# Performance work log

Measured on AMD Instinct MI355X. Metric: run time of the kernel, lower is better.

## Reference

```python
import jax, jax.numpy as jnp
import numpy as np

S, C, HD = 2048, 3072, 128
H = C // HD  # 24 heads
EPS = 1e-6


def setup_inputs() -> dict:
    key = jax.random.key(0)
    ks = jax.random.split(key, 12)
    x = jax.random.normal(ks[0], (S, C), dtype=jnp.float32)
    rope = jax.random.normal(ks[1], (S, 1, HD // 2, 2, 2), dtype=jnp.float32)
    w = 0.02
    return {
        "x": x,
        "rope": rope,
        "wq": jax.random.normal(ks[2], (C, C), dtype=jnp.float32) * w,
        "bq": jnp.zeros((C,), dtype=jnp.float32),
        "wk": jax.random.normal(ks[3], (C, C), dtype=jnp.float32) * w,
        "bk": jnp.zeros((C,), dtype=jnp.float32),
        "wv": jax.random.normal(ks[4], (C, C), dtype=jnp.float32) * w,
        "bv": jnp.zeros((C,), dtype=jnp.float32),
        "wo": jax.random.normal(ks[5], (C, C), dtype=jnp.float32) * w,
        "bo": jnp.zeros((C,), dtype=jnp.float32),
        "qn_w": jnp.ones((HD,), dtype=jnp.float32),
        "kn_w": jnp.ones((HD,), dtype=jnp.float32),
    }


def _rmsnorm(t, w):
    # t: [S, H, HD]; normalize over last dim
    ms = jnp.mean(t * t, axis=-1, keepdims=True)
    return t * jax.lax.rsqrt(ms + EPS) * w


def _apply_rotary(t, rope):
    # t: [S, H, HD] -> [S, H, HD//2, 1, 2]; rope: [S, 1, HD//2, 2, 2]
    t_ = t.reshape(S, H, HD // 2, 1, 2)
    out = jnp.sum(rope * t_, axis=-1)  # [S, H, HD//2, 2]
    return out.reshape(S, H, HD)


def reference(x, rope, wq, bq, wk, bk, wv, bv, wo, bo, qn_w, kn_w):
    q = (x @ wq.T + bq).reshape(S, H, HD)
    k = (x @ wk.T + bk).reshape(S, H, HD)
    v = (x @ wv.T + bv).reshape(S, H, HD)
    q = _rmsnorm(q, qn_w)
    k = _rmsnorm(k, kn_w)
    q = _apply_rotary(q, rope)
    k = _apply_rotary(k, rope)
    # dense SDPA: scores [H, S, S]
    scores = jnp.einsum('shd,thd->hst', q, k) / jnp.sqrt(jnp.float32(HD))
    attn = jax.nn.softmax(scores, axis=-1)
    out = jnp.einsum('hst,thd->shd', attn, v).reshape(S, C)
    return out @ wo.T + bo
```

## Files before the change

### kernel.cpp

```cpp
#include <hip/hip_runtime.h>
#include <cstdint>
#include <cstddef>

#define SS 2048
#define CC 3072
#define HDIM 128
#define NH 24

using bf16 = __bf16;
typedef __bf16 bf16x8 __attribute__((ext_vector_type(8)));
typedef float f32x4 __attribute__((ext_vector_type(4)));

typedef const __attribute__((address_space(1))) void* gas1_cvp;
typedef __attribute__((address_space(3))) void* las3_vp;

__device__ __forceinline__ void gll16(const void* g, void* l) {
  __builtin_amdgcn_global_load_lds((gas1_cvp)g, (las3_vp)l, 16, 0, 0);
}

__device__ __forceinline__ bf16x8 cvt8(f32x4 a, f32x4 b) {
  bf16x8 r;
  r[0] = (bf16)a[0]; r[1] = (bf16)a[1]; r[2] = (bf16)a[2]; r[3] = (bf16)a[3];
  r[4] = (bf16)b[0]; r[5] = (bf16)b[1]; r[6] = (bf16)b[2]; r[7] = (bf16)b[3];
  return r;
}

#define NX ((size_t)SS * CC)
#define NW ((size_t)CC * CC)

__global__ __launch_bounds__(256)
void k_cvt(const float* __restrict__ s0, const float* __restrict__ s1,
           const float* __restrict__ s2, const float* __restrict__ s3,
           const float* __restrict__ s4, bf16* __restrict__ dst) {
  const int z = blockIdx.y;
  const float* src = (z == 0) ? s0 : (z == 1) ? s1 : (z == 2) ? s2 : (z == 3) ? s3 : s4;
  const size_t nz = (z == 0) ? NX : NW;
  const size_t base = (z == 0) ? 0 : NX + (size_t)(z - 1) * NW;
  const size_t i = ((size_t)blockIdx.x * 256 + threadIdx.x) * 8;
  if (i < nz) {
    const f32x4 a = *(const f32x4*)(src + i);
    const f32x4 b = *(const f32x4*)(src + i + 4);
    *(bf16x8*)(dst + base + i) = cvt8(a, b);
  }
}

__device__ __forceinline__ void gemm_bt_bf16(const bf16* __restrict__ A,
                                             const bf16* __restrict__ W,
                                             const float* __restrict__ bias,
                                             void* __restrict__ out,
                                             int M, int N, int K, int mode) {
  __shared__ __align__(16) bf16 As[2][128][32];
  __shared__ __align__(16) bf16 Ws[2][128][32];
  const int t = threadIdx.x, wave = t >> 6, lane = t & 63;
  const int m0 = blockIdx.y * 128, n0 = blockIdx.x * 128;
  const int wm = (wave >> 1) * 64, wn = (wave & 1) * 64;
  const int fr = lane & 15, fq = (lane >> 4) * 8;

  f32x4 acc[4][4] = {};

  for (int k0 = 0; k0 < K; k0 += 64) {
    __syncthreads();
#pragma unroll
    for (int it = 0; it < 4; ++it) {
      const int pc = wave * 4 + it;
      const int pl = pc >> 3, rb = pc & 7;
      const int row = rb * 16 + (lane >> 2);
      const int c8 = (lane & 3) * 8;
      gll16(A + (size_t)(m0 + row) * K + k0 + pl * 32 + c8,
            (char*)&As[0][0][0] + pc * 1024);
      gll16(W + (size_t)(n0 + row) * K + k0 + pl * 32 + c8,
            (char*)&Ws[0][0][0] + pc * 1024);
    }
    __syncthreads();
#pragma unroll
    for (int c = 0; c < 2; ++c) {
      bf16x8 a[4], b[4];
#pragma unroll
      for (int i = 0; i < 4; ++i) a[i] = *(const bf16x8*)&As[c][wm + i * 16 + fr][fq];
#pragma unroll
      for (int j = 0; j < 4; ++j) b[j] = *(const bf16x8*)&Ws[c][wn + j * 16 + fr][fq];
#pragma unroll
      for (int i = 0; i < 4; ++i)
#pragma unroll
        for (int j = 0; j < 4; ++j)
          acc[i][j] = __builtin_amdgcn_mfma_f32_16x16x32_bf16(a[i], b[j], acc[i][j], 0, 0, 0);
    }
  }

  const int lr4 = (lane >> 4) * 4;
#pragma unroll
  for (int i = 0; i < 4; ++i) {
#pragma unroll
    for (int j = 0; j < 4; ++j) {
      const int col = n0 + wn + j * 16 + fr;
      const float bb = bias[col];
#pragma unroll
      for (int r = 0; r < 4; ++r) {
        const int row = m0 + wm + i * 16 + lr4 + r;
        const float v = acc[i][j][r] + bb;
        if (mode == 0)
          ((bf16*)out)[((size_t)(col >> 7) * M + row) * 128 + (col & 127)] = (bf16)v;
        else if (mode == 1)
          ((bf16*)out)[(size_t)col * M + row] = (bf16)v;
        else
          ((float*)out)[(size_t)row * N + col] = v;
      }
    }
  }
}

__global__ __launch_bounds__(256, 4)
void k_gemm_qkv_b(const bf16* __restrict__ xb,
                  const bf16* __restrict__ wqb, const bf16* __restrict__ wkb,
                  const bf16* __restrict__ wvb,
                  const float* __restrict__ bq, const float* __restrict__ bk,
                  const float* __restrict__ bv,
                  bf16* __restrict__ Qo, bf16* __restrict__ Ko, bf16* __restrict__ Vo) {
  const int z = blockIdx.z;
  const bf16* W  = (z == 0) ? wqb : (z == 1) ? wkb : wvb;
  const float* B = (z == 0) ? bq : (z == 1) ? bk : bv;
  void* O        = (z == 0) ? (void*)Qo : (z == 1) ? (void*)Ko : (void*)Vo;
  gemm_bt_bf16(xb, W, B, O, SS, CC, CC, (z == 2) ? 1 : 0);
}

__global__ __launch_bounds__(256, 4)
void k_gemm_out_b(const bf16* __restrict__ A, const bf16* __restrict__ wob,
                  const float* __restrict__ bo, float* __restrict__ out) {
  gemm_bt_bf16(A, wob, bo, out, SS, CC, CC, 2);
}

template<int AF32>
__device__ __forceinline__ void gemm_core(const void* __restrict__ Ap,
                                          const float* __restrict__ W,
                                          const float* __restrict__ bias,
                                          void* __restrict__ out,
                                          int M, int N, int K, int mode) {
  __shared__ __align__(16) bf16 As[128][32];
  __shared__ __align__(16) bf16 Ws[128][32];
  const int t = threadIdx.x, wave = t >> 6, lane = t & 63;
  const int m0 = blockIdx.y * 128, n0 = blockIdx.x * 128;
  const int wm = (wave >> 1) * 64, wn = (wave & 1) * 64;
  const int fr = lane & 15, fq = (lane >> 4) * 8;
  const int pi0 = wave * 128 + lane;
  const int pi1 = pi0 + 64;
  const int row0 = pi0 >> 2, c0 = (pi0 & 3) * 8;
  const int row1 = pi1 >> 2, c1 = (pi1 & 3) * 8;

  f32x4 raf0[2], raf1[2], rw0[2], rw1[2];
  bf16x8 rab0, rab1;

  auto issue = [&](int k0) {
    if (AF32) {
      const float* A = (const float*)Ap;
      const float* p0 = A + (size_t)(m0 + row0) * K + k0 + c0;
      raf0[0] = *(const f32x4*)p0; raf0[1] = *(const f32x4*)(p0 + 4);
      const float* p1 = A + (size_t)(m0 + row1) * K + k0 + c1;
      raf1[0] = *(const f32x4*)p1; raf1[1] = *(const f32x4*)(p1 + 4);
    } else {
      const bf16* A = (const bf16*)Ap;
      rab0 = *(const bf16x8*)(A + (size_t)(m0 + row0) * K + k0 + c0);
      rab1 = *(const bf16x8*)(A + (size_t)(m0 + row1) * K + k0 + c1);
    }
    const float* q0 = W + (size_t)(n0 + row0) * K + k0 + c0;
    rw0[0] = *(const f32x4*)q0; rw0[1] = *(const f32x4*)(q0 + 4);
    const float* q1 = W + (size_t)(n0 + row1) * K + k0 + c1;
    rw1[0] = *(const f32x4*)q1; rw1[1] = *(const f32x4*)(q1 + 4);
  };

  f32x4 acc[4][4] = {};
  issue(0);
  for (int k0 = 0; k0 < K; k0 += 32) {
    __syncthreads();
    if (AF32) {
      *(bf16x8*)&As[row0][c0] = cvt8(raf0[0], raf0[1]);
      *(bf16x8*)&As[row1][c1] = cvt8(raf1[0], raf1[1]);
    } else {
      *(bf16x8*)&As[row0][c0] = rab0;
      *(bf16x8*)&As[row1][c1] = rab1;
    }
    *(bf16x8*)&Ws[row0][c0] = cvt8(rw0[0], rw0[1]);
    *(bf16x8*)&Ws[row1][c1] = cvt8(rw1[0], rw1[1]);
    __syncthreads();
    if (k0 + 32 < K) issue(k0 + 32);
    bf16x8 a[4], b[4];
#pragma unroll
    for (int i = 0; i < 4; ++i) a[i] = *(const bf16x8*)&As[wm + i * 16 + fr][fq];
#pragma unroll
    for (int j = 0; j < 4; ++j) b[j] = *(const bf16x8*)&Ws[wn + j * 16 + fr][fq];
#pragma unroll
    for (int i = 0; i < 4; ++i)
#pragma unroll
      for (int j = 0; j < 4; ++j)
        acc[i][j] = __builtin_amdgcn_mfma_f32_16x16x32_bf16(a[i], b[j], acc[i][j], 0, 0, 0);
  }

  const int lr4 = (lane >> 4) * 4;
#pragma unroll
  for (int i = 0; i < 4; ++i) {
#pragma unroll
    for (int j = 0; j < 4; ++j) {
      const int col = n0 + wn + j * 16 + fr;
      const float bb = bias[col];
#pragma unroll
      for (int r = 0; r < 4; ++r) {
        const int row = m0 + wm + i * 16 + lr4 + r;
        const float v = acc[i][j][r] + bb;
        if (mode == 0)
          ((bf16*)out)[((size_t)(col >> 7) * M + row) * 128 + (col & 127)] = (bf16)v;
        else if (mode == 1)
          ((bf16*)out)[(size_t)col * M + row] = (bf16)v;
        else
          ((float*)out)[(size_t)row * N + col] = v;
      }
    }
  }
}

__global__ __launch_bounds__(256, 2)
void k_gemm_qkv_f(const float* __restrict__ x,
                  const float* __restrict__ wq, const float* __restrict__ wk,
                  const float* __restrict__ wv,
                  const float* __restrict__ bq, const float* __restrict__ bk,
                  const float* __restrict__ bv,
                  bf16* __restrict__ Qo, bf16* __restrict__ Ko, bf16* __restrict__ Vo) {
  const int z = blockIdx.z;
  const float* W = (z == 0) ? wq : (z == 1) ? wk : wv;
  const float* B = (z == 0) ? bq : (z == 1) ? bk : bv;
  void* O        = (z == 0) ? (void*)Qo : (z == 1) ? (void*)Ko : (void*)Vo;
  gemm_core<1>(x, W, B, O, SS, CC, CC, (z == 2) ? 1 : 0);
}

__global__ __launch_bounds__(256, 2)
void k_gemm_out_f(const bf16* __restrict__ A, const float* __restrict__ wo,
                  const float* __restrict__ bo, float* __restrict__ out) {
  gemm_core<0>(A, wo, bo, out, SS, CC, CC, 2);
}

__global__ __launch_bounds__(256)
void k_norm_rope(bf16* __restrict__ Q, bf16* __restrict__ K,
                 const float* __restrict__ rope,
                 const float* __restrict__ qw, const float* __restrict__ kw) {
  const int t = threadIdx.x, wave = t >> 6, lane = t & 63;
  const int idx = blockIdx.x * 4 + wave;
  const int s = idx / NH, h = idx % NH;
  const size_t base = ((size_t)h * SS + s) * HDIM + 2 * lane;

  bf16 q2[2], k2[2];
  *(uint32_t*)q2 = *(const uint32_t*)(Q + base);
  *(uint32_t*)k2 = *(const uint32_t*)(K + base);
  const float q0 = (float)q2[0], q1 = (float)q2[1];
  const float k0 = (float)k2[0], k1 = (float)k2[1];
  float sq = q0 * q0 + q1 * q1;
  float sk = k0 * k0 + k1 * k1;
#pragma unroll
  for (int m = 1; m < 64; m <<= 1) {
    sq += __shfl_xor(sq, m);
    sk += __shfl_xor(sk, m);
  }
  const float rq = rsqrtf(sq * (1.0f / 128.0f) + 1e-6f);
  const float rk = rsqrtf(sk * (1.0f / 128.0f) + 1e-6f);

  const float qn0 = q0 * rq * qw[2 * lane], qn1 = q1 * rq * qw[2 * lane + 1];
  const float kn0 = k0 * rk * kw[2 * lane], kn1 = k1 * rk * kw[2 * lane + 1];

  const f32x4 rp = *(const f32x4*)(rope + (size_t)s * 256 + 4 * lane);
  const float r00 = rp[0], r01 = rp[1], r10 = rp[2], r11 = rp[3];

  const float SC = 0.08838834764831845f * 1.44269504088896340f;
  const float oq0 = (r00 * qn0 + r01 * qn1) * SC;
  const float oq1 = (r10 * qn0 + r11 * qn1) * SC;
  const float ok0 = r00 * kn0 + r01 * kn1;
  const float ok1 = r10 * kn0 + r11 * kn1;

  bf16 wq2[2] = {(bf16)oq0, (bf16)oq1};
  bf16 wk2[2] = {(bf16)ok0, (bf16)ok1};
  *(uint32_t*)(Q + base) = *(uint32_t*)wq2;
  *(uint32_t*)(K + base) = *(uint32_t*)wk2;
}

__global__ __launch_bounds__(128, 2)
void k_attn(const bf16* __restrict__ Q, const bf16* __restrict__ Kt,
            const bf16* __restrict__ Vt, bf16* __restrict__ Out) {
  __shared__ __align__(16) bf16 Ks[2][64][128];
  __shared__ __align__(16) bf16 Vs[128][64];
  const int t = threadIdx.x, wave = t >> 6, lane = t & 63;
  const int bx = blockIdx.x;
  const int xg = bx & 7, slot = bx >> 3;
  const int h = xg * 3 + (slot >> 5);
  const int q0 = (slot & 31) * 64;
  const int fr = lane & 15, fq = (lane >> 4) * 8;
  const int g4 = lane >> 4;
  const int wq0 = wave * 32;
  const float FM = 32.0f;

  bf16x8 aq[2][4];
#pragma unroll
  for (int qt = 0; qt < 2; ++qt)
#pragma unroll
    for (int kc = 0; kc < 4; ++kc)
      aq[qt][kc] = *(const bf16x8*)(
          Q + ((size_t)h * SS + q0 + wq0 + qt * 16 + fr) * HDIM + kc * 32 + fq);

  auto stageK = [&](int buf, int k0) {
#pragma unroll
    for (int it = 0; it < 8; ++it) {
      const int pc = wave * 8 + it;
      const int s  = pc * 4 + (lane >> 4);
      const int kp = 32 * ((s >> 4) & 1) + 8 * ((s >> 2) & 3)
                   + 4 * (s >> 5) + (s & 3);
      const int sl = (lane & 15) ^ (s & 7);
      gll16(Kt + ((size_t)h * SS + k0 + kp) * HDIM + sl * 8,
            (char*)&Ks[buf][0][0] + pc * 1024);
    }
  };
  auto stageV = [&](int k0) {
#pragma unroll
    for (int it = 0; it < 8; ++it) {
      const int pc = wave * 8 + it;
      const int d  = pc * 8 + (lane >> 3);
      const int sl = (lane & 7) ^ (d & 7);
      gll16(Vt + ((size_t)h * HDIM + d) * SS + k0 + sl * 8,
            (char*)&Vs[0][0] + pc * 1024);
    }
  };

  f32x4 oacc[2][8] = {};
  float lacc[2] = {0.f, 0.f};

  stageK(0, 0);
  int cur = 0;

  for (int k0 = 0; k0 < SS; k0 += 64) {
    const bool notlast = (k0 + 64 < SS);
    stageV(k0);
    if (notlast) {
      stageK(cur ^ 1, k0 + 64);
      asm volatile("s_waitcnt vmcnt(16)" ::: "memory");
    } else {
      asm volatile("s_waitcnt vmcnt(8)" ::: "memory");
    }
    __builtin_amdgcn_s_barrier();
    __builtin_amdgcn_sched_barrier(0);

    f32x4 sacc[2][4] = {};
#pragma unroll
    for (int kc = 0; kc < 4; ++kc) {
#pragma unroll
      for (int jt = 0; jt < 4; ++jt) {
        const bf16x8 b =
            *(const bf16x8*)&Ks[cur][jt * 16 + fr][((((kc << 2) + g4) ^ (fr & 7)) << 3)];
        sacc[0][jt] = __builtin_amdgcn_mfma_f32_16x16x32_bf16(b, aq[0][kc], sacc[0][jt], 0, 0, 0);
        sacc[1][jt] = __builtin_amdgcn_mfma_f32_16x16x32_bf16(b, aq[1][kc], sacc[1][jt], 0, 0, 0);
      }
    }

    bf16x8 ap[2][2];
#pragma unroll
    for (int qt = 0; qt < 2; ++qt) {
      float pv[4][4];
      float ps = 0.f;
#pragma unroll
      for (int jt = 0; jt < 4; ++jt)
#pragma unroll
        for (int r = 0; r < 4; ++r) {
          pv[jt][r] = exp2f(sacc[qt][jt][r] - FM);
          ps += pv[jt][r];
        }
      lacc[qt] += ps;
#pragma unroll
      for (int kc = 0; kc < 2; ++kc) {
        bf16x8 a;
        a[0] = (bf16)pv[kc][0];     a[1] = (bf16)pv[kc][1];
        a[2] = (bf16)pv[kc][2];     a[3] = (bf16)pv[kc][3];
        a[4] = (bf16)pv[2 + kc][0]; a[5] = (bf16)pv[2 + kc][1];
        a[6] = (bf16)pv[2 + kc][2]; a[7] = (bf16)pv[2 + kc][3];
        ap[qt][kc] = a;
      }
    }

    if (notlast) {
      asm volatile("s_waitcnt vmcnt(8)" ::: "memory");
    } else {
      asm volatile("s_waitcnt vmcnt(0)" ::: "memory");
    }
    __builtin_amdgcn_s_barrier();
    __builtin_amdgcn_sched_barrier(0);

#pragma unroll
    for (int kc = 0; kc < 2; ++kc) {
#pragma unroll
      for (int jd = 0; jd < 8; ++jd) {
        const int d = jd * 16 + fr;
        const bf16x8 b =
            *(const bf16x8*)&Vs[d][((((kc << 2) + g4) ^ (fr & 7)) << 3)];
        oacc[0][jd] = __builtin_amdgcn_mfma_f32_16x16x32_bf16(ap[0][kc], b, oacc[0][jd], 0, 0, 0);
        oacc[1][jd] = __builtin_amdgcn_mfma_f32_16x16x32_bf16(ap[1][kc], b, oacc[1][jd], 0, 0, 0);
      }
    }

    __builtin_amdgcn_s_barrier();
    __builtin_amdgcn_sched_barrier(0);
    cur ^= 1;
  }

#pragma unroll
  for (int qt = 0; qt < 2; ++qt) {
    float l = lacc[qt];
    l += __shfl_xor(l, 16);
    l += __shfl_xor(l, 32);
    const float linv = 1.0f / l;
#pragma unroll
    for (int r = 0; r < 4; ++r) {
      const float inv = __shfl(linv, g4 * 4 + r, 16);
      const int row = q0 + wq0 + qt * 16 + g4 * 4 + r;
#pragma unroll
      for (int jd = 0; jd < 8; ++jd) {
        const int col = h * HDIM + jd * 16 + fr;
        Out[(size_t)row * CC + col] = (bf16)(oacc[qt][jd][r] * inv);
      }
    }
  }
}

extern "C" void kernel_launch(void* const* d_in, const int* in_sizes, int n_in,
                              void* d_out, int out_size, void* d_ws, size_t ws_size,
                              hipStream_t stream) {
  const float* x    = (const float*)d_in[0];
  const float* rope = (const float*)d_in[1];
  const float* wq   = (const float*)d_in[2];
  const float* bq   = (const float*)d_in[3];
  const float* wk   = (const float*)d_in[4];
  const float* bk   = (const float*)d_in[5];
  const float* wv   = (const float*)d_in[6];
  const float* bv   = (const float*)d_in[7];
  const float* wo   = (const float*)d_in[8];
  const float* bo   = (const float*)d_in[9];
  const float* qw   = (const float*)d_in[10];
  const float* kw   = (const float*)d_in[11];

  const size_t need = (4 * NX + 4 * NW) * sizeof(bf16);
  bf16* Vt = (bf16*)d_out;

  if (ws_size >= need) {
    bf16* xb  = (bf16*)d_ws;
    bf16* wqb = xb + NX;
    bf16* wkb = wqb + NW;
    bf16* wvb = wkb + NW;
    bf16* wob = wvb + NW;
    bf16* Qn  = wob + NW;
    bf16* Kn  = Qn + NX;
    bf16* Ao  = Kn + NX;

    k_cvt<<<dim3((unsigned)(NW / 2048), 5), 256, 0, stream>>>(x, wq, wk, wv, wo, xb);
    k_gemm_qkv_b<<<dim3(CC / 128, SS / 128, 3), 256, 0, stream>>>(
        xb, wqb, wkb, wvb, bq, bk, bv, Qn, Kn, Vt);
    k_norm_rope<<<dim3(SS * NH / 4), 256, 0, stream>>>(Qn, Kn, rope, qw, kw);
    k_attn<<<dim3((SS / 64) * NH), 128, 0, stream>>>(Qn, Kn, Vt, Ao);
    k_gemm_out_b<<<dim3(CC / 128, SS / 128), 256, 0, stream>>>(Ao, wob, bo, (float*)d_out);
  } else {
    bf16* Qn = (bf16*)d_ws;
    bf16* Kn = Qn + NX;
    bf16* Ao = Kn + NX;

    k_gemm_qkv_f<<<dim3(CC / 128, SS / 128, 3), 256, 0, stream>>>(
        x, wq, wk, wv, bq, bk, bv, Qn, Kn, Vt);
    k_norm_rope<<<dim3(SS * NH / 4), 256, 0, stream>>>(Qn, Kn, rope, qw, kw);
    k_attn<<<dim3((SS / 64) * NH), 128, 0, stream>>>(Qn, Kn, Vt, Ao);
    k_gemm_out_f<<<dim3(CC / 128, SS / 128), 256, 0, stream>>>(Ao, wo, bo, (float*)d_out);
  }
}
```

Measured before the change: 508.9 us.

## Replace QKV GEMM with 256x256-tile, 8-wave, XOR-swizzled, double-buffered kernel

Adds a new QKV projection kernel that uses 256x256 output tiles with 512 threads (8 waves), 64-wide K steps, XOR-swizzled LDS layout, and interleaves next-tile global-to-LDS loads with MFMA phases under raised wave priority. Larger tiles raise arithmetic intensity and cut redundant global reads. The swizzle avoids LDS bank conflicts. The cost is a big LDS footprint (128KB), high register use for the 8x4 accumulators, and only 288 blocks, which may leave compute units unevenly loaded.

```diff
diff --git a/kernel.cpp b/kernel.cpp
--- a/kernel.cpp
+++ b/kernel.cpp
@@ -44,6 +44,105 @@
   }
 }
 
+__global__ __launch_bounds__(512, 2)
+void k_gemm_qkv_8p(const bf16* __restrict__ xb,
+                   const bf16* __restrict__ wqb, const bf16* __restrict__ wkb,
+                   const bf16* __restrict__ wvb,
+                   const float* __restrict__ bq, const float* __restrict__ bk,
+                   const float* __restrict__ bv,
+                   bf16* __restrict__ Qo, bf16* __restrict__ Ko, bf16* __restrict__ Vo) {
+  const int z = blockIdx.z;
+  const bf16* W   = (z == 0) ? wqb : (z == 1) ? wkb : wvb;
+  const float* Bi = (z == 0) ? bq : (z == 1) ? bk : bv;
+  const int mode  = (z == 2) ? 1 : 0;
+  void* out       = (z == 0) ? (void*)Qo : (z == 1) ? (void*)Ko : (void*)Vo;
+
+  __shared__ __align__(16) bf16 As[2][256][64];
+  __shared__ __align__(16) bf16 Ws[2][256][64];
+  const int t = threadIdx.x, wave = t >> 6, lane = t & 63;
+  const int m0 = blockIdx.y * 256, n0 = blockIdx.x * 256;
+  const int wm = (wave >> 2) * 128, wn = (wave & 3) * 64;
+  const int fr = lane & 15, g4 = lane >> 4;
+  const int K = CC, M = SS;
+
+  auto stage = [&](int buf, int k0, int i) {
+    const int c = wave * 4 + i;
+    const int row = c * 8 + (lane >> 3);
+    const int sl = (lane & 7) ^ (row & 7);
+    gll16(xb + (size_t)(m0 + row) * K + k0 + sl * 8,
+          (char*)&As[buf][0][0] + c * 1024);
+    gll16(W + (size_t)(n0 + row) * K + k0 + sl * 8,
+          (char*)&Ws[buf][0][0] + c * 1024);
+  };
+
+  f32x4 acc[8][4] = {};
+
+  stage(0, 0, 0); stage(0, 0, 1); stage(0, 0, 2); stage(0, 0, 3);
+
+  const int NT = K / 64;
+  for (int tt = 0; tt < NT; ++tt) {
+    const int buf = tt & 1;
+    asm volatile("s_waitcnt vmcnt(0)" ::: "memory");
+    __builtin_amdgcn_s_barrier();
+    __builtin_amdgcn_sched_barrier(0);
+
+    bf16x8 bfr[4][2];
+#pragma unroll
+    for (int ni = 0; ni < 4; ++ni)
+#pragma unroll
+      for (int kk = 0; kk < 2; ++kk) {
+        const int row = wn + ni * 16 + fr;
+        const int sl = (kk * 4 + g4) ^ (row & 7);
+        bfr[ni][kk] = *(const bf16x8*)((const char*)&Ws[buf][0][0] + row * 128 + sl * 16);
+      }
+
+#pragma unroll
+    for (int ph = 0; ph < 4; ++ph) {
+      bf16x8 am[2][2];
+#pragma unroll
+      for (int mi2 = 0; mi2 < 2; ++mi2)
+#pragma unroll
+        for (int kk = 0; kk < 2; ++kk) {
+          const int row = wm + (ph * 2 + mi2) * 16 + fr;
+          const int sl = (kk * 4 + g4) ^ (row & 7);
+          am[mi2][kk] = *(const bf16x8*)((const char*)&As[buf][0][0] + row * 128 + sl * 16);
+        }
+      if (ph < 2 && tt + 1 < NT) {
+        stage(buf ^ 1, (tt + 1) * 64, ph * 2);
+        stage(buf ^ 1, (tt + 1) * 64, ph * 2 + 1);
+      }
+      __builtin_amdgcn_s_setprio(1);
+#pragma unroll
+      for (int kk = 0; kk < 2; ++kk)
+#pragma unroll
+        for (int mi2 = 0; mi2 < 2; ++mi2)
+#pragma unroll
+          for (int ni = 0; ni < 4; ++ni)
+            acc[ph * 2 + mi2][ni] = __builtin_amdgcn_mfma_f32_16x16x32_bf16(
+                am[mi2][kk], bfr[ni][kk], acc[ph * 2 + mi2][ni], 0, 0, 0);
+      __builtin_amdgcn_s_setprio(0);
+    }
+  }
+
+  const int lr4 = g4 * 4;
+#pragma unroll
+  for (int mi = 0; mi < 8; ++mi)
+#pragma unroll
+    for (int ni = 0; ni < 4; ++ni) {
+      const int col = n0 + wn + ni * 16 + fr;
+      const float bb = Bi[col];
+#pragma unroll
+      for (int r = 0; r < 4; ++r) {
+        const int row = m0 + wm + mi * 16 + lr4 + r;
+        const float v = acc[mi][ni][r] + bb;
+        if (mode == 0)
+          ((bf16*)out)[((size_t)(col >> 7) * M + row) * 128 + (col & 127)] = (bf16)v;
+        else
+          ((bf16*)out)[(size_t)col * M + row] = (bf16)v;
+      }
+    }
+}
+
 __device__ __forceinline__ void gemm_bt_bf16(const bf16* __restrict__ A,
                                              const bf16* __restrict__ W,
                                              const float* __restrict__ bias,
@@ -107,20 +206,6 @@
       }
     }
   }
-}
-
-__global__ __launch_bounds__(256, 4)
-void k_gemm_qkv_b(const bf16* __restrict__ xb,
-                  const bf16* __restrict__ wqb, const bf16* __restrict__ wkb,
-                  const bf16* __restrict__ wvb,
-                  const float* __restrict__ bq, const float* __restrict__ bk,
-                  const float* __restrict__ bv,
-                  bf16* __restrict__ Qo, bf16* __restrict__ Ko, bf16* __restrict__ Vo) {
-  const int z = blockIdx.z;
-  const bf16* W  = (z == 0) ? wqb : (z == 1) ? wkb : wvb;
-  const float* B = (z == 0) ? bq : (z == 1) ? bk : bv;
-  void* O        = (z == 0) ? (void*)Qo : (z == 1) ? (void*)Ko : (void*)Vo;
-  gemm_bt_bf16(xb, W, B, O, SS, CC, CC, (z == 2) ? 1 : 0);
 }
 
 __global__ __launch_bounds__(256, 4)
@@ -452,7 +537,7 @@
     bf16* Ao  = Kn + NX;
 
     k_cvt<<<dim3((unsigned)(NW / 2048), 5), 256, 0, stream>>>(x, wq, wk, wv, wo, xb);
-    k_gemm_qkv_b<<<dim3(CC / 128, SS / 128, 3), 256, 0, stream>>>(
+    k_gemm_qkv_8p<<<dim3(CC / 256, SS / 256, 3), 512, 0, stream>>>(
         xb, wqb, wkb, wvb, bq, bk, bv, Qn, Kn, Vt);
     k_norm_rope<<<dim3(SS * NH / 4), 256, 0, stream>>>(Qn, Kn, rope, qw, kw);
     k_attn<<<dim3((SS / 64) * NH), 128, 0, stream>>>(Qn, Kn, Vt, Ao);
```

Measured after the change: 545.3 us. 7.1% more time.

## Fuse RMSNorm and rotary embedding into QKV GEMM epilogue

Applied to the files above, without the earlier changes.

Moves the per-head RMSNorm, rotary application and Q scaling into the epilogue of the bf16 QKV GEMM, so the separate norm/rope kernel launch is dropped on the workspace path. Row sums of squares are reduced across lanes with shuffles, and partial sums from the two N-waves are combined through a small shared array, since each 128-column tile is exactly one head. This removes a full read-modify-write pass over Q and K. In exchange it adds epilogue work, extra rope loads per element and a block barrier inside the GEMM.

```diff
diff --git a/kernel.cpp b/kernel.cpp
--- a/kernel.cpp
+++ b/kernel.cpp
@@ -27,6 +27,7 @@
 
 #define NX ((size_t)SS * CC)
 #define NW ((size_t)CC * CC)
+#define QSCALE (0.08838834764831845f * 1.44269504088896340f)
 
 __global__ __launch_bounds__(256)
 void k_cvt(const float* __restrict__ s0, const float* __restrict__ s1,
@@ -48,9 +49,13 @@
                                              const bf16* __restrict__ W,
                                              const float* __restrict__ bias,
                                              void* __restrict__ out,
-                                             int M, int N, int K, int mode) {
+                                             int M, int N, int K, int mode,
+                                             const float* __restrict__ nw,
+                                             const float* __restrict__ rope_t,
+                                             float scale) {
   __shared__ __align__(16) bf16 As[2][128][32];
   __shared__ __align__(16) bf16 Ws[2][128][32];
+  __shared__ float rs_[4][64];
   const int t = threadIdx.x, wave = t >> 6, lane = t & 63;
   const int m0 = blockIdx.y * 128, n0 = blockIdx.x * 128;
   const int wm = (wave >> 1) * 64, wn = (wave & 1) * 64;
@@ -88,6 +93,60 @@
   }
 
   const int lr4 = (lane >> 4) * 4;
+
+  if (mode == 0) {
+    float bcol[4], nwv[4];
+#pragma unroll
+    for (int j = 0; j < 4; ++j) {
+      bcol[j] = bias[n0 + wn + j * 16 + fr];
+      nwv[j]  = nw[wn + j * 16 + fr];
+    }
+    float ss[4][4];
+#pragma unroll
+    for (int i = 0; i < 4; ++i)
+#pragma unroll
+      for (int r = 0; r < 4; ++r) {
+        float s = 0.f;
+#pragma unroll
+        for (int j = 0; j < 4; ++j) {
+          const float v = acc[i][j][r] + bcol[j];
+          s += v * v;
+        }
+#pragma unroll
+        for (int m = 1; m < 16; m <<= 1) s += __shfl_xor(s, m);
+        ss[i][r] = s;
+      }
+    if (fr == 0) {
+#pragma unroll
+      for (int i = 0; i < 4; ++i)
+#pragma unroll
+        for (int r = 0; r < 4; ++r)
+          rs_[wave][i * 16 + lr4 + r] = ss[i][r];
+    }
+    __syncthreads();
+
+    const int hh = n0 >> 7;
+#pragma unroll
+    for (int i = 0; i < 4; ++i)
+#pragma unroll
+      for (int r = 0; r < 4; ++r) {
+        const float tot = ss[i][r] + rs_[wave ^ 1][i * 16 + lr4 + r];
+        const float rq = rsqrtf(tot * (1.0f / 128.0f) + 1e-6f);
+        const int srow = m0 + wm + i * 16 + lr4 + r;
+#pragma unroll
+        for (int j = 0; j < 4; ++j) {
+          const int d = wn + j * 16 + fr;
+          const float vn = (acc[i][j][r] + bcol[j]) * rq * nwv[j];
+          const float vp = __shfl_xor(vn, 1);
+          const f32x4 rp = *(const f32x4*)(rope_t + (size_t)srow * 256 + (d >> 1) * 4);
+          const float o = ((d & 1) ? (rp[2] * vp + rp[3] * vn)
+                                   : (rp[0] * vn + rp[1] * vp)) * scale;
+          ((bf16*)out)[((size_t)hh * M + srow) * 128 + d] = (bf16)o;
+        }
+      }
+    return;
+  }
+
 #pragma unroll
   for (int i = 0; i < 4; ++i) {
 #pragma unroll
@@ -98,9 +157,7 @@
       for (int r = 0; r < 4; ++r) {
         const int row = m0 + wm + i * 16 + lr4 + r;
         const float v = acc[i][j][r] + bb;
-        if (mode == 0)
-          ((bf16*)out)[((size_t)(col >> 7) * M + row) * 128 + (col & 127)] = (bf16)v;
-        else if (mode == 1)
+        if (mode == 1)
           ((bf16*)out)[(size_t)col * M + row] = (bf16)v;
         else
           ((float*)out)[(size_t)row * N + col] = v;
@@ -115,18 +172,22 @@
                   const bf16* __restrict__ wvb,
                   const float* __restrict__ bq, const float* __restrict__ bk,
                   const float* __restrict__ bv,
+                  const float* __restrict__ rope,
+                  const float* __restrict__ qw, const float* __restrict__ kw,
                   bf16* __restrict__ Qo, bf16* __restrict__ Ko, bf16* __restrict__ Vo) {
   const int z = blockIdx.z;
-  const bf16* W  = (z == 0) ? wqb : (z == 1) ? wkb : wvb;
-  const float* B = (z == 0) ? bq : (z == 1) ? bk : bv;
-  void* O        = (z == 0) ? (void*)Qo : (z == 1) ? (void*)Ko : (void*)Vo;
-  gemm_bt_bf16(xb, W, B, O, SS, CC, CC, (z == 2) ? 1 : 0);
+  if (z == 0)
+    gemm_bt_bf16(xb, wqb, bq, Qo, SS, CC, CC, 0, qw, rope, QSCALE);
+  else if (z == 1)
+    gemm_bt_bf16(xb, wkb, bk, Ko, SS, CC, CC, 0, kw, rope, 1.0f);
+  else
+    gemm_bt_bf16(xb, wvb, bv, Vo, SS, CC, CC, 1, nullptr, nullptr, 1.0f);
 }
 
 __global__ __launch_bounds__(256, 4)
 void k_gemm_out_b(const bf16* __restrict__ A, const bf16* __restrict__ wob,
                   const float* __restrict__ bo, float* __restrict__ out) {
-  gemm_bt_bf16(A, wob, bo, out, SS, CC, CC, 2);
+  gemm_bt_bf16(A, wob, bo, out, SS, CC, CC, 2, nullptr, nullptr, 1.0f);
 }
 
 template<int AF32>
@@ -266,9 +327,8 @@
   const f32x4 rp = *(const f32x4*)(rope + (size_t)s * 256 + 4 * lane);
   const float r00 = rp[0], r01 = rp[1], r10 = rp[2], r11 = rp[3];
 
-  const float SC = 0.08838834764831845f * 1.44269504088896340f;
-  const float oq0 = (r00 * qn0 + r01 * qn1) * SC;
-  const float oq1 = (r10 * qn0 + r11 * qn1) * SC;
+  const float oq0 = (r00 * qn0 + r01 * qn1) * QSCALE;
+  const float oq1 = (r10 * qn0 + r11 * qn1) * QSCALE;
   const float ok0 = r00 * kn0 + r01 * kn1;
   const float ok1 = r10 * kn0 + r11 * kn1;
 
@@ -453,8 +513,7 @@
 
     k_cvt<<<dim3((unsigned)(NW / 2048), 5), 256, 0, stream>>>(x, wq, wk, wv, wo, xb);
     k_gemm_qkv_b<<<dim3(CC / 128, SS / 128, 3), 256, 0, stream>>>(
-        xb, wqb, wkb, wvb, bq, bk, bv, Qn, Kn, Vt);
-    k_norm_rope<<<dim3(SS * NH / 4), 256, 0, stream>>>(Qn, Kn, rope, qw, kw);
+        xb, wqb, wkb, wvb, bq, bk, bv, rope, qw, kw, Qn, Kn, Vt);
     k_attn<<<dim3((SS / 64) * NH), 128, 0, stream>>>(Qn, Kn, Vt, Ao);
     k_gemm_out_b<<<dim3(CC / 128, SS / 128), 256, 0, stream>>>(Ao, wob, bo, (float*)d_out);
   } else {
```

After: 487.3 us. 1.04x faster.
